# Performance work log

Hardware: AMD Instinct MI355X
Metric: run time of the kernel (lower is better)

The kernel has to match this reference:

```python
import jax, jax.numpy as jnp
import numpy as np

B, N, DIM = 8, 1024, 512
HEADS, DIM_HEAD = 8, 64
INNER = HEADS * DIM_HEAD  # 512
SCALE = DIM_HEAD ** -0.5
EPS = 1e-5


def setup_inputs() -> dict:
    key = jax.random.key(0)
    k = jax.random.split(key, 6)
    x = jax.random.normal(k[0], (B, N, DIM), dtype=jnp.float32)
    gamma = jnp.ones((DIM,), dtype=jnp.float32)
    beta = jnp.zeros((DIM,), dtype=jnp.float32)
    # Linear weights stored as (in, out) so y = x @ W (equivalent to torch x @ W.T)
    W_qk = jax.random.normal(k[1], (DIM, 2 * INNER), dtype=jnp.float32) * (DIM ** -0.5)
    W_v = jax.random.normal(k[2], (DIM, INNER), dtype=jnp.float32) * (DIM ** -0.5)
    W_out = jax.random.normal(k[3], (INNER, DIM), dtype=jnp.float32) * (INNER ** -0.5)
    return {"x": x, "gamma": gamma, "beta": beta, "W_qk": W_qk, "W_v": W_v, "W_out": W_out}


def _layernorm(x, gamma, beta):
    mu = jnp.mean(x, axis=-1, keepdims=True)
    var = jnp.mean(jnp.square(x - mu), axis=-1, keepdims=True)
    return (x - mu) * jax.lax.rsqrt(var + EPS) * gamma + beta


def reference(x, gamma, beta, W_qk, W_v, W_out):
    xn = _layernorm(x, gamma, beta)                       # [B,N,D]
    v = xn @ W_v                                          # [B,N,INNER]
    qk = xn @ W_qk                                        # [B,N,2*INNER]
    q, k = jnp.split(qk, 2, axis=-1)
    # b n (h d) -> b h n d
    q = q.reshape(B, N, HEADS, DIM_HEAD).transpose(0, 2, 1, 3)
    k = k.reshape(B, N, HEADS, DIM_HEAD).transpose(0, 2, 1, 3)
    vh = v.reshape(B, N, HEADS, DIM_HEAD).transpose(0, 2, 1, 3)
    dots = jnp.einsum('bhnd,bhmd->bhnm', q, k) * SCALE    # [B,H,N,N]
    attn = jax.nn.softmax(dots, axis=-1)
    out = jnp.einsum('bhnm,bhmd->bhnd', attn, vh)         # [B,H,N,d]
    out = out.transpose(0, 2, 1, 3).reshape(B, N, INNER)  # b h n d -> b n (h d)
    return out @ W_out                                    # [B,N,DIM]
```

## Files before the change

### kernel.cpp

```cpp
#include <hip/hip_runtime.h>

#define TOK 8192
#define DMODEL 512
#define SEQ 1024
#define NH 8
#define DH 64

typedef _Float16 half8 __attribute__((ext_vector_type(8)));
typedef _Float16 half4v __attribute__((ext_vector_type(4)));
typedef float floatx4 __attribute__((ext_vector_type(4)));

__device__ __forceinline__ void gll16(const void* g, void* l) {
  __builtin_amdgcn_global_load_lds(
      (const __attribute__((address_space(1))) void*)g,
      (__attribute__((address_space(3))) void*)l, 16, 0, 0);
}

__global__ __launch_bounds__(256) void prep_kernel(
    const float* __restrict__ x, const float* __restrict__ gamma,
    const float* __restrict__ beta, _Float16* __restrict__ xn,
    const float* __restrict__ Wqk, const float* __restrict__ Wv,
    const float* __restrict__ Wo, _Float16* __restrict__ WqkvT,
    _Float16* __restrict__ WoutT) {
  __shared__ float t[32][33];
  const int bid = blockIdx.x;
  if (bid < 2048) {
    const int row = bid * 4 + (threadIdx.x >> 6);
    const int tt = threadIdx.x & 63;
    const float* xr = x + (size_t)row * DMODEL;
    const float4 a = *(const float4*)(xr + tt * 4);
    const float4 b = *(const float4*)(xr + 256 + tt * 4);
    float s  = a.x + a.y + a.z + a.w + b.x + b.y + b.z + b.w;
    float ss = a.x*a.x + a.y*a.y + a.z*a.z + a.w*a.w
             + b.x*b.x + b.y*b.y + b.z*b.z + b.w*b.w;
    #pragma unroll
    for (int m = 1; m < 64; m <<= 1) {
      s  += __shfl_xor(s, m);
      ss += __shfl_xor(ss, m);
    }
    const float mean = s * (1.0f / DMODEL);
    const float var  = ss * (1.0f / DMODEL) - mean * mean;
    const float inv  = rsqrtf(var + 1e-5f);
    const float4 g0  = *(const float4*)(gamma + tt * 4);
    const float4 g1  = *(const float4*)(gamma + 256 + tt * 4);
    const float4 be0 = *(const float4*)(beta + tt * 4);
    const float4 be1 = *(const float4*)(beta + 256 + tt * 4);
    half4v o0, o1;
    o0[0] = (_Float16)((a.x - mean) * inv * g0.x + be0.x);
    o0[1] = (_Float16)((a.y - mean) * inv * g0.y + be0.y);
    o0[2] = (_Float16)((a.z - mean) * inv * g0.z + be0.z);
    o0[3] = (_Float16)((a.w - mean) * inv * g0.w + be0.w);
    o1[0] = (_Float16)((b.x - mean) * inv * g1.x + be1.x);
    o1[1] = (_Float16)((b.y - mean) * inv * g1.y + be1.y);
    o1[2] = (_Float16)((b.z - mean) * inv * g1.z + be1.z);
    o1[3] = (_Float16)((b.w - mean) * inv * g1.w + be1.w);
    _Float16* outr = xn + (size_t)row * DMODEL;
    *(half4v*)(outr + tt * 4) = o0;
    *(half4v*)(outr + 256 + tt * 4) = o1;
  } else {
    const int r = bid - 2048;
    const int z = r >> 9;
    const int rem = r & 511;
    const float* W;
    _Float16* dst;
    int N, rowoff;
    if (z == 0)      { W = Wqk; dst = WqkvT; N = 1024; rowoff = 0; }
    else if (z == 1) { W = Wv;  dst = WqkvT; N = 512;  rowoff = 1024; }
    else             { W = Wo;  dst = WoutT; N = 512;  rowoff = 0; }
    const int n0 = (rem & 31) * 32;
    if (n0 >= N) return;
    const int k0 = (rem >> 5) * 32;
    const int tx = threadIdx.x & 31, ty = threadIdx.x >> 5;
    #pragma unroll
    for (int j = 0; j < 4; ++j)
      t[ty + j * 8][tx] = W[(size_t)(k0 + ty + j * 8) * N + n0 + tx];
    __syncthreads();
    #pragma unroll
    for (int j = 0; j < 4; ++j)
      dst[(size_t)(rowoff + n0 + ty + j * 8) * 512 + k0 + tx] =
          (_Float16)t[tx][ty + j * 8];
  }
}

__global__ __launch_bounds__(256) void hgemm_qkv(
    const _Float16* __restrict__ A, const _Float16* __restrict__ Bt,
    _Float16* __restrict__ Q, _Float16* __restrict__ V, int K) {
  __shared__ char smem[49152];
  const int tid = threadIdx.x;
  const int bm = blockIdx.x, bn = blockIdx.y;
  const int wv = tid >> 6, lane = tid & 63;
  const int l15 = lane & 15, g = lane >> 4;
  const int wr = wv >> 1, wc = wv & 1;
  const _Float16* Ab = A + (size_t)(bm * 128) * K;
  const _Float16* Bb = Bt + (size_t)(bn * 128) * K;
  const int lrow = lane >> 2;
  const int lchk = (lane & 3) * 16;
  const int ssw = lchk ^ (((lrow >> 1) & 3) << 4);

  #define HG_STAGE(buf, kt)                                                   \
    _Pragma("unroll")                                                         \
    for (int i = 0; i < 2; ++i) {                                             \
      const int rbase = wv * 16 + i * 64;                                     \
      gll16((const char*)(Ab + (size_t)(rbase + lrow) * K + (kt)) + ssw,      \
            smem + (buf) * 16384 + rbase * 64);                               \
      gll16((const char*)(Bb + (size_t)(rbase + lrow) * K + (kt)) + ssw,      \
            smem + (buf) * 16384 + 8192 + rbase * 64);                        \
    }

  floatx4 acc[4][4] = {};
  HG_STAGE(0, 0);
  HG_STAGE(1, 32);
  int cur = 0;
  const int nit = K >> 5;
  for (int it = 0; it < nit; ++it) {
    if (it < nit - 2) asm volatile("s_waitcnt vmcnt(4)" ::: "memory");
    else              asm volatile("s_waitcnt vmcnt(0)" ::: "memory");
    __builtin_amdgcn_s_barrier();
    asm volatile("" ::: "memory");
    const int nxt = cur + 2 >= 3 ? cur - 1 : cur + 2;
    if (it + 2 < nit) { HG_STAGE(nxt, (it + 2) * 32); }
    const char* sb = smem + cur * 16384;
    half8 af[4], bf[4];
    #pragma unroll
    for (int mt = 0; mt < 4; ++mt) {
      const int row = wr * 64 + mt * 16 + l15;
      af[mt] = *(const half8*)(sb + row * 64 +
                               ((g * 16) ^ (((row >> 1) & 3) << 4)));
    }
    #pragma unroll
    for (int nt = 0; nt < 4; ++nt) {
      const int row = wc * 64 + nt * 16 + l15;
      bf[nt] = *(const half8*)(sb + 8192 + row * 64 +
                               ((g * 16) ^ (((row >> 1) & 3) << 4)));
    }
    __builtin_amdgcn_s_setprio(1);
    #pragma unroll
    for (int mt = 0; mt < 4; ++mt)
      #pragma unroll
      for (int nt = 0; nt < 4; ++nt)
        acc[mt][nt] = __builtin_amdgcn_mfma_f32_16x16x32_f16(
            af[mt], bf[nt], acc[mt][nt], 0, 0, 0);
    __builtin_amdgcn_s_setprio(0);
    cur = cur + 1 >= 3 ? 0 : cur + 1;
  }
  #undef HG_STAGE
  const int m0 = bm * 128 + wr * 64;
  const int n0 = bn * 128 + wc * 64;
  #pragma unroll
  for (int mt = 0; mt < 4; ++mt) {
    const int mrow = m0 + mt * 16 + 4 * g;
    const int b = mrow >> 10, tok = mrow & 1023;
    #pragma unroll
    for (int nt = 0; nt < 4; ++nt) {
      const int n = n0 + nt * 16 + l15;
      if (n < 1024) {
        #pragma unroll
        for (int r = 0; r < 4; ++r)
          Q[(size_t)(mrow + r) * 1024 + n] = (_Float16)acc[mt][nt][r];
      } else {
        const int cv = n - 1024;
        half4v hv;
        #pragma unroll
        for (int r = 0; r < 4; ++r) hv[r] = (_Float16)acc[mt][nt][r];
        *(half4v*)(V + ((size_t)((b * 8 + (cv >> 6)) * 64 + (cv & 63)) << 10) + tok) = hv;
      }
    }
  }
}

__global__ __launch_bounds__(512) void hgemm_out(
    const _Float16* __restrict__ A, const _Float16* __restrict__ Bt,
    float* __restrict__ C) {
  __shared__ char smem[49152];
  const int tid = threadIdx.x;
  const int bm = blockIdx.x, bn = blockIdx.y;
  const int wv = tid >> 6, lane = tid & 63;
  const int l15 = lane & 15, g = lane >> 4;
  const int wr = wv >> 2, wc = wv & 3;
  const _Float16* Ab = A + (size_t)(bm * 128) * 512;
  const _Float16* Bb = Bt + (size_t)(bn * 128) * 512;
  const int lrow = lane >> 2;
  const int lchk = (lane & 3) * 16;
  const int ssw = lchk ^ (((lrow >> 1) & 3) << 4);

  #define OUT_STAGE(buf, kt)                                                  \
    {                                                                         \
      gll16((const char*)(Ab + (size_t)(wv * 16 + lrow) * 512 + (kt)) + ssw,  \
            smem + (buf) * 16384 + wv * 16 * 64);                             \
      gll16((const char*)(Bb + (size_t)(wv * 16 + lrow) * 512 + (kt)) + ssw,  \
            smem + (buf) * 16384 + 8192 + wv * 16 * 64);                      \
    }

  floatx4 acc[4][2] = {};
  OUT_STAGE(0, 0);
  OUT_STAGE(1, 32);
  int cur = 0;
  for (int it = 0; it < 16; ++it) {
    if (it < 14) asm volatile("s_waitcnt vmcnt(2)" ::: "memory");
    else         asm volatile("s_waitcnt vmcnt(0)" ::: "memory");
    __builtin_amdgcn_s_barrier();
    asm volatile("" ::: "memory");
    const int nxt = cur + 2 >= 3 ? cur - 1 : cur + 2;
    if (it + 2 < 16) { OUT_STAGE(nxt, (it + 2) * 32); }
    const char* sb = smem + cur * 16384;
    half8 af[4], bf[2];
    #pragma unroll
    for (int mt = 0; mt < 4; ++mt) {
      const int row = wr * 64 + mt * 16 + l15;
      af[mt] = *(const half8*)(sb + row * 64 +
                               ((g * 16) ^ (((row >> 1) & 3) << 4)));
    }
    #pragma unroll
    for (int nt = 0; nt < 2; ++nt) {
      const int row = wc * 32 + nt * 16 + l15;
      bf[nt] = *(const half8*)(sb + 8192 + row * 64 +
                               ((g * 16) ^ (((row >> 1) & 3) << 4)));
    }
    __builtin_amdgcn_s_setprio(1);
    #pragma unroll
    for (int mt = 0; mt < 4; ++mt)
      #pragma unroll
      for (int nt = 0; nt < 2; ++nt)
        acc[mt][nt] = __builtin_amdgcn_mfma_f32_16x16x32_f16(
            af[mt], bf[nt], acc[mt][nt], 0, 0, 0);
    __builtin_amdgcn_s_setprio(0);
    cur = cur + 1 >= 3 ? 0 : cur + 1;
  }
  #undef OUT_STAGE
  const int m0 = bm * 128 + wr * 64;
  const int n0 = bn * 128 + wc * 32;
  #pragma unroll
  for (int mt = 0; mt < 4; ++mt)
    #pragma unroll
    for (int nt = 0; nt < 2; ++nt) {
      const int n = n0 + nt * 16 + l15;
      #pragma unroll
      for (int r = 0; r < 4; ++r)
        C[(size_t)(m0 + mt * 16 + 4 * g + r) * 512 + n] = acc[mt][nt][r];
    }
}

#define QSC 0.18033688f
#define MOFF 5.7707801f

__global__ __launch_bounds__(256) void flash16_kernel(
    const _Float16* __restrict__ qkh, const _Float16* __restrict__ vt,
    _Float16* __restrict__ ao) {
  __shared__ char smem[65536];
  const int bh = blockIdx.x;
  const int qt = blockIdx.y;
  const int b = bh >> 3, h = bh & 7;
  const int tid = threadIdx.x;
  const int wv = tid >> 6, lane = tid & 63;
  const int l15 = lane & 15, g = lane >> 4;
  const int swz = (l15 & 7) << 4;
  const int qrow0 = b * SEQ + qt * 128;
  const int qbase = qrow0 + wv * 32;

  half8 qf[2][2];
  #pragma unroll
  for (int grp = 0; grp < 2; ++grp) {
    const _Float16* qp = qkh + (size_t)(qbase + grp * 16 + l15) * 1024 + h * DH;
    qf[grp][0] = *(const half8*)(qp + g * 8);
    qf[grp][1] = *(const half8*)(qp + g * 8 + 32);
    qf[grp][0] *= (_Float16)QSC;
    qf[grp][1] *= (_Float16)QSC;
  }

  float lsum[2] = {0.f, 0.f};
  floatx4 oacc[2][4] = {};

  const int lrow = lane >> 3;
  const int lchk = (lane & 7) * 16;
  const int ssw = lchk ^ (lrow << 4);
  const _Float16* kbase = qkh + 512 + h * DH;
  const _Float16* vbase = vt + (size_t)bh * 64 * 1024;
  char* pb = smem + 49152 + wv * 4096 + l15 * 128;

  #define FL_STAGE(buf, kt)                                                   \
    _Pragma("unroll")                                                         \
    for (int i = 0; i < 2; ++i) {                                             \
      const int rr = i * 32 + wv * 8;                                         \
      gll16((const char*)(kbase +                                             \
            (size_t)(b * SEQ + (kt) * 64 + rr + lrow) * 1024) + ssw,          \
            smem + (buf) * 16384 + rr * 128);                                 \
      gll16((const char*)(vbase + (size_t)(rr + lrow) * 1024 +                \
            (kt) * 64) + ssw,                                                 \
            smem + (buf) * 16384 + 8192 + rr * 128);                          \
    }

  FL_STAGE(0, 0);
  FL_STAGE(1, 1);
  int cur = 0;
  for (int kt = 0; kt < 16; ++kt) {
    if (kt < 15) asm volatile("s_waitcnt vmcnt(4)" ::: "memory");
    else         asm volatile("s_waitcnt vmcnt(0)" ::: "memory");
    __builtin_amdgcn_s_barrier();
    asm volatile("" ::: "memory");
    const int nxt = cur + 2 >= 3 ? cur - 1 : cur + 2;
    if (kt + 2 < 16) FL_STAGE(nxt, kt + 2);
    const char* sb = smem + cur * 16384;

    floatx4 sacc[2][4] = {};
    __builtin_amdgcn_s_setprio(1);
    #pragma unroll
    for (int kk = 0; kk < 2; ++kk) {
      #pragma unroll
      for (int mt = 0; mt < 4; ++mt) {
        half8 af = *(const half8*)(sb + (16 * mt + l15) * 128 +
                                   ((g * 16 + kk * 64) ^ swz));
        sacc[0][mt] = __builtin_amdgcn_mfma_f32_16x16x32_f16(af, qf[0][kk], sacc[0][mt], 0, 0, 0);
        sacc[1][mt] = __builtin_amdgcn_mfma_f32_16x16x32_f16(af, qf[1][kk], sacc[1][mt], 0, 0, 0);
      }
    }
    __builtin_amdgcn_s_setprio(0);

    #pragma unroll
    for (int grp = 0; grp < 2; ++grp) {
      float rsp[4];
      #pragma unroll
      for (int mt = 0; mt < 4; ++mt) {
        float p0 = exp2f(sacc[grp][mt][0] - MOFF);
        float p1 = exp2f(sacc[grp][mt][1] - MOFF);
        float p2 = exp2f(sacc[grp][mt][2] - MOFF);
        float p3 = exp2f(sacc[grp][mt][3] - MOFF);
        rsp[mt] = (p0 + p1) + (p2 + p3);
        half4v pv;
        pv[0] = (_Float16)p0; pv[1] = (_Float16)p1;
        pv[2] = (_Float16)p2; pv[3] = (_Float16)p3;
        *(half4v*)(pb + grp * 2048 + ((32 * mt + 8 * g) ^ swz)) = pv;
      }
      float rs = (rsp[0] + rsp[1]) + (rsp[2] + rsp[3]);
      rs += __shfl_xor(rs, 16);
      rs += __shfl_xor(rs, 32);
      lsum[grp] += rs;
    }

    __builtin_amdgcn_s_setprio(1);
    #pragma unroll
    for (int kk = 0; kk < 2; ++kk) {
      half8 pf0 = *(const half8*)(pb + ((g * 16 + kk * 64) ^ swz));
      half8 pf1 = *(const half8*)(pb + 2048 + ((g * 16 + kk * 64) ^ swz));
      #pragma unroll
      for (int mt = 0; mt < 4; ++mt) {
        half8 vf = *(const half8*)(sb + 8192 + (16 * mt + l15) * 128 +
                                   ((g * 16 + kk * 64) ^ swz));
        oacc[0][mt] = __builtin_amdgcn_mfma_f32_16x16x32_f16(vf, pf0, oacc[0][mt], 0, 0, 0);
        oacc[1][mt] = __builtin_amdgcn_mfma_f32_16x16x32_f16(vf, pf1, oacc[1][mt], 0, 0, 0);
      }
    }
    __builtin_amdgcn_s_setprio(0);
    cur = cur + 1 >= 3 ? 0 : cur + 1;
  }
  #undef FL_STAGE

  #pragma unroll
  for (int grp = 0; grp < 2; ++grp) {
    const float inv = 1.0f / lsum[grp];
    _Float16* op = ao + (size_t)(qbase + grp * 16 + l15) * 512 + h * DH;
    #pragma unroll
    for (int mt = 0; mt < 4; ++mt) {
      half4v hv;
      hv[0] = (_Float16)(oacc[grp][mt][0] * inv);
      hv[1] = (_Float16)(oacc[grp][mt][1] * inv);
      hv[2] = (_Float16)(oacc[grp][mt][2] * inv);
      hv[3] = (_Float16)(oacc[grp][mt][3] * inv);
      *(half4v*)(op + 16 * mt + 4 * g) = hv;
    }
  }
}

extern "C" void kernel_launch(void* const* d_in, const int* in_sizes, int n_in,
                              void* d_out, int out_size, void* d_ws, size_t ws_size,
                              hipStream_t stream) {
  const float* x     = (const float*)d_in[0];
  const float* gamma = (const float*)d_in[1];
  const float* beta  = (const float*)d_in[2];
  const float* W_qk  = (const float*)d_in[3];
  const float* W_v   = (const float*)d_in[4];
  const float* W_out = (const float*)d_in[5];
  float* out = (float*)d_out;
  char* ws = (char*)d_ws;

  const size_t MB = 1024 * 1024;
  _Float16* xn16  = (_Float16*)ws;
  _Float16* qkh   = (_Float16*)(ws + 8 * MB);
  _Float16* vt    = (_Float16*)(ws + 24 * MB);
  _Float16* ao16  = (_Float16*)(ws + 32 * MB);
  _Float16* WqkvT = (_Float16*)(ws + 40 * MB);
  _Float16* WoutT = (_Float16*)(ws + 42 * MB);

  prep_kernel<<<3584, 256, 0, stream>>>(x, gamma, beta, xn16,
                                        W_qk, W_v, W_out, WqkvT, WoutT);
  hgemm_qkv<<<dim3(64, 12), 256, 0, stream>>>(xn16, WqkvT, qkh, vt, 512);
  flash16_kernel<<<dim3(64, 8), 256, 0, stream>>>(qkh, vt, ao16);
  hgemm_out<<<dim3(64, 4), 512, 0, stream>>>(ao16, WoutT, out);
}
```

Before: 80.78 us.

## Split flash attention key tiles across two wave groups with LDS reduction

The attention kernel now launches 512 threads per block. Each of 4 query-row wave pairs splits every 64-key tile into two halves handled by separate waves, and the partial output accumulators and row sums are combined through shared memory at the end. This doubles the waves available to hide latency and halves per-wave MFMA and exp work per tile, with only one load per operand per thread per stage. The cost is an extra LDS reduction epilogue, two more barriers, and higher register pressure per block.

```diff
diff --git a/kernel.cpp b/kernel.cpp
--- a/kernel.cpp
+++ b/kernel.cpp
@@ -243,7 +243,7 @@
 #define QSC 0.18033688f
 #define MOFF 5.7707801f
 
-__global__ __launch_bounds__(256) void flash16_kernel(
+__global__ __launch_bounds__(512) void flash16_kernel(
     const _Float16* __restrict__ qkh, const _Float16* __restrict__ vt,
     _Float16* __restrict__ ao) {
   __shared__ char smem[65536];
@@ -254,8 +254,10 @@
   const int wv = tid >> 6, lane = tid & 63;
   const int l15 = lane & 15, g = lane >> 4;
   const int swz = (l15 & 7) << 4;
+  const int qq = wv & 3;
+  const int khalf = wv >> 2;
   const int qrow0 = b * SEQ + qt * 128;
-  const int qbase = qrow0 + wv * 32;
+  const int qbase = qrow0 + qq * 32;
 
   half8 qf[2][2];
   #pragma unroll
@@ -275,25 +277,23 @@
   const int ssw = lchk ^ (lrow << 4);
   const _Float16* kbase = qkh + 512 + h * DH;
   const _Float16* vbase = vt + (size_t)bh * 64 * 1024;
-  char* pb = smem + 49152 + wv * 4096 + l15 * 128;
+  char* pb = smem + 49152 + wv * 2048 + l15 * 128;
 
   #define FL_STAGE(buf, kt)                                                   \
-    _Pragma("unroll")                                                         \
-    for (int i = 0; i < 2; ++i) {                                             \
-      const int rr = i * 32 + wv * 8;                                         \
-      gll16((const char*)(kbase +                                             \
-            (size_t)(b * SEQ + (kt) * 64 + rr + lrow) * 1024) + ssw,          \
-            smem + (buf) * 16384 + rr * 128);                                 \
-      gll16((const char*)(vbase + (size_t)(rr + lrow) * 1024 +                \
-            (kt) * 64) + ssw,                                                 \
-            smem + (buf) * 16384 + 8192 + rr * 128);                          \
+    {                                                                         \
+      const int krow = b * SEQ + (kt) * 64 + wv * 8 + lrow;                   \
+      gll16((const char*)(kbase + (size_t)krow * 1024) + ssw,                 \
+            smem + (buf) * 16384 + wv * 1024);                                \
+      gll16((const char*)(vbase + (size_t)(wv * 8 + lrow) * 1024 +            \
+                          (kt) * 64) + ssw,                                   \
+            smem + (buf) * 16384 + 8192 + wv * 1024);                         \
     }
 
   FL_STAGE(0, 0);
   FL_STAGE(1, 1);
   int cur = 0;
   for (int kt = 0; kt < 16; ++kt) {
-    if (kt < 15) asm volatile("s_waitcnt vmcnt(4)" ::: "memory");
+    if (kt < 15) asm volatile("s_waitcnt vmcnt(2)" ::: "memory");
     else         asm volatile("s_waitcnt vmcnt(0)" ::: "memory");
     __builtin_amdgcn_s_barrier();
     asm volatile("" ::: "memory");
@@ -301,13 +301,13 @@
     if (kt + 2 < 16) FL_STAGE(nxt, kt + 2);
     const char* sb = smem + cur * 16384;
 
-    floatx4 sacc[2][4] = {};
+    floatx4 sacc[2][2] = {};
     __builtin_amdgcn_s_setprio(1);
     #pragma unroll
     for (int kk = 0; kk < 2; ++kk) {
       #pragma unroll
-      for (int mt = 0; mt < 4; ++mt) {
-        half8 af = *(const half8*)(sb + (16 * mt + l15) * 128 +
+      for (int mt = 0; mt < 2; ++mt) {
+        half8 af = *(const half8*)(sb + (khalf * 32 + mt * 16 + l15) * 128 +
                                    ((g * 16 + kk * 64) ^ swz));
         sacc[0][mt] = __builtin_amdgcn_mfma_f32_16x16x32_f16(af, qf[0][kk], sacc[0][mt], 0, 0, 0);
         sacc[1][mt] = __builtin_amdgcn_mfma_f32_16x16x32_f16(af, qf[1][kk], sacc[1][mt], 0, 0, 0);
@@ -317,9 +317,9 @@
 
     #pragma unroll
     for (int grp = 0; grp < 2; ++grp) {
-      float rsp[4];
-      #pragma unroll
-      for (int mt = 0; mt < 4; ++mt) {
+      float rsp[2];
+      #pragma unroll
+      for (int mt = 0; mt < 2; ++mt) {
         float p0 = exp2f(sacc[grp][mt][0] - MOFF);
         float p1 = exp2f(sacc[grp][mt][1] - MOFF);
         float p2 = exp2f(sacc[grp][mt][2] - MOFF);
@@ -328,44 +328,68 @@
         half4v pv;
         pv[0] = (_Float16)p0; pv[1] = (_Float16)p1;
         pv[2] = (_Float16)p2; pv[3] = (_Float16)p3;
-        *(half4v*)(pb + grp * 2048 + ((32 * mt + 8 * g) ^ swz)) = pv;
+        *(half4v*)(pb + ((grp * 64 + 32 * mt + 8 * g) ^ swz)) = pv;
       }
-      float rs = (rsp[0] + rsp[1]) + (rsp[2] + rsp[3]);
+      float rs = rsp[0] + rsp[1];
       rs += __shfl_xor(rs, 16);
       rs += __shfl_xor(rs, 32);
       lsum[grp] += rs;
     }
 
     __builtin_amdgcn_s_setprio(1);
-    #pragma unroll
-    for (int kk = 0; kk < 2; ++kk) {
-      half8 pf0 = *(const half8*)(pb + ((g * 16 + kk * 64) ^ swz));
-      half8 pf1 = *(const half8*)(pb + 2048 + ((g * 16 + kk * 64) ^ swz));
-      #pragma unroll
-      for (int mt = 0; mt < 4; ++mt) {
-        half8 vf = *(const half8*)(sb + 8192 + (16 * mt + l15) * 128 +
-                                   ((g * 16 + kk * 64) ^ swz));
-        oacc[0][mt] = __builtin_amdgcn_mfma_f32_16x16x32_f16(vf, pf0, oacc[0][mt], 0, 0, 0);
-        oacc[1][mt] = __builtin_amdgcn_mfma_f32_16x16x32_f16(vf, pf1, oacc[1][mt], 0, 0, 0);
-      }
+    half8 pf0 = *(const half8*)(pb + ((g * 16) ^ swz));
+    half8 pf1 = *(const half8*)(pb + ((64 + g * 16) ^ swz));
+    #pragma unroll
+    for (int dt = 0; dt < 4; ++dt) {
+      half8 vf = *(const half8*)(sb + 8192 + (dt * 16 + l15) * 128 +
+                                 ((khalf * 64 + g * 16) ^ swz));
+      oacc[0][dt] = __builtin_amdgcn_mfma_f32_16x16x32_f16(vf, pf0, oacc[0][dt], 0, 0, 0);
+      oacc[1][dt] = __builtin_amdgcn_mfma_f32_16x16x32_f16(vf, pf1, oacc[1][dt], 0, 0, 0);
     }
     __builtin_amdgcn_s_setprio(0);
     cur = cur + 1 >= 3 ? 0 : cur + 1;
   }
   #undef FL_STAGE
 
-  #pragma unroll
-  for (int grp = 0; grp < 2; ++grp) {
-    const float inv = 1.0f / lsum[grp];
-    _Float16* op = ao + (size_t)(qbase + grp * 16 + l15) * 512 + h * DH;
-    #pragma unroll
-    for (int mt = 0; mt < 4; ++mt) {
-      half4v hv;
-      hv[0] = (_Float16)(oacc[grp][mt][0] * inv);
-      hv[1] = (_Float16)(oacc[grp][mt][1] * inv);
-      hv[2] = (_Float16)(oacc[grp][mt][2] * inv);
-      hv[3] = (_Float16)(oacc[grp][mt][3] * inv);
-      *(half4v*)(op + 16 * mt + 4 * g) = hv;
+  __syncthreads();
+  float* red = (float*)smem;
+  if (wv >= 4) {
+    const int idx = ((wv - 4) * 64 + lane) * 34;
+    #pragma unroll
+    for (int grp = 0; grp < 2; ++grp)
+      #pragma unroll
+      for (int dt = 0; dt < 4; ++dt)
+        #pragma unroll
+        for (int r = 0; r < 4; ++r)
+          red[idx + grp * 16 + dt * 4 + r] = oacc[grp][dt][r];
+    red[idx + 32] = lsum[0];
+    red[idx + 33] = lsum[1];
+  }
+  __syncthreads();
+  if (wv < 4) {
+    const int idx = (wv * 64 + lane) * 34;
+    #pragma unroll
+    for (int grp = 0; grp < 2; ++grp)
+      #pragma unroll
+      for (int dt = 0; dt < 4; ++dt)
+        #pragma unroll
+        for (int r = 0; r < 4; ++r)
+          oacc[grp][dt][r] += red[idx + grp * 16 + dt * 4 + r];
+    lsum[0] += red[idx + 32];
+    lsum[1] += red[idx + 33];
+    #pragma unroll
+    for (int grp = 0; grp < 2; ++grp) {
+      const float inv = 1.0f / lsum[grp];
+      _Float16* op = ao + (size_t)(qbase + grp * 16 + l15) * 512 + h * DH;
+      #pragma unroll
+      for (int dt = 0; dt < 4; ++dt) {
+        half4v hv;
+        hv[0] = (_Float16)(oacc[grp][dt][0] * inv);
+        hv[1] = (_Float16)(oacc[grp][dt][1] * inv);
+        hv[2] = (_Float16)(oacc[grp][dt][2] * inv);
+        hv[3] = (_Float16)(oacc[grp][dt][3] * inv);
+        *(half4v*)(op + dt * 16 + 4 * g) = hv;
+      }
     }
   }
 }
@@ -393,6 +417,6 @@
   prep_kernel<<<3584, 256, 0, stream>>>(x, gamma, beta, xn16,
                                         W_qk, W_v, W_out, WqkvT, WoutT);
   hgemm_qkv<<<dim3(64, 12), 256, 0, stream>>>(xn16, WqkvT, qkh, vt, 512);
-  flash16_kernel<<<dim3(64, 8), 256, 0, stream>>>(qkh, vt, ao16);
+  flash16_kernel<<<dim3(64, 8), 512, 0, stream>>>(qkh, vt, ao16);
   hgemm_out<<<dim3(64, 4), 512, 0, stream>>>(ao16, WoutT, out);
 }
```

After: 75.27 us. -6.8%, faster.
